# Kernel tuning notes

Measured on AMD Instinct MI355X. Metric: run time of the kernel, lower is better.

The kernel has to match this reference:

```python
import jax, jax.numpy as jnp
import numpy as np

NUM_CLASSES = 19
VIEWS = 50          # views_per_class: min(min_views, max_views_per_class)=50, no max_features_total cap (38*50<=10000)
TEMP = 0.1
CM_TEMP = 0.1
EPS = 1e-12


def setup_inputs() -> dict:
    key = jax.random.key(0)
    k1, k2, k3 = jax.random.split(key, 3)
    label = jax.random.randint(k1, (2, 512, 1024), 0, NUM_CLASSES)
    color_fea = jax.random.normal(k2, (2, 256, 128, 256), dtype=jnp.float32)
    other_fea = jax.random.normal(k3, (2, 256, 128, 256), dtype=jnp.float32)
    return {"label": label, "color_fea": color_fea, "other_fea": other_fea}


def _sample(compare, feature):
    # compare: [N, Cc, HW] bool (pixel belongs to class), feature: [N, C, HW]
    # random per-class sampling of VIEWS pixels: argsort random keys restricted to class pixels
    n, cc, hw = compare.shape
    rand = jax.random.uniform(jax.random.key(42), (n, hw))
    keys = jnp.where(compare, rand[:, None, :], 2.0)          # non-class pixels pushed to the end
    idx = jnp.argsort(keys, axis=-1)[:, :, :VIEWS]            # [N, Cc, V]
    samp = jnp.take_along_axis(feature[:, None, :, :], idx[:, :, None, :], axis=-1)  # [N, Cc, C, V]
    c = feature.shape[1]
    return samp.reshape(n * cc, c, VIEWS)                     # [T, C, V]


def _norm_flat(feats):
    # feats: [T, C, V] -> l2-normalize over C, transpose, flatten to [T*V, C]
    f = feats / jnp.maximum(jnp.linalg.norm(feats, axis=1, keepdims=True), EPS)
    t, c, v = f.shape
    return jnp.transpose(f, (0, 2, 1)).reshape(t * v, c)


def _masks(labels_flat):
    m = (labels_flat[:, None] == labels_flat[None, :]).astype(jnp.float32)
    neg = 1.0 - m
    pos = m * (1.0 - jnp.eye(m.shape[0], dtype=m.dtype))      # exclude self from positives
    return pos, neg


def _infonce(dot, pos, neg):
    exp = jnp.exp(dot)
    neg_logits = (exp * neg).sum(1, keepdims=True)
    log_prob = dot - jnp.log(exp + neg_logits)
    pos_sums = pos.sum(1)
    norm = jnp.where(pos_sums > 0, pos_sums, 1.0)
    return -(((pos * log_prob).sum(1)) / norm).mean()


def reference(label, color_fea, other_fea):
    n, h, w = label.shape
    scale = w // color_fea.shape[-1]
    # nearest-neighbour downsample of label to feature resolution (torch interpolate 'nearest' with integer factor)
    ld = label[:, ::scale, ::scale].reshape(n, -1)                       # [N, HW]
    compare = ld[:, None, :] == jnp.arange(NUM_CLASSES)[None, :, None]   # [N, Cc, HW]
    cf = color_fea.reshape(n, color_fea.shape[1], -1)
    of = other_fea.reshape(n, other_fea.shape[1], -1)
    fc = _sample(compare, cf)                                            # [T, C, V]
    fo = _sample(compare, of)
    labels = jnp.tile(jnp.arange(NUM_CLASSES), n).astype(jnp.float32)    # [T]
    labels_flat = jnp.repeat(labels, VIEWS)                              # [T*V]
    pos, neg = _masks(labels_flat)
    fcf = _norm_flat(fc)
    fof = _norm_flat(fo)
    loss_cm = _infonce(fcf @ fof.T / CM_TEMP, pos, neg)
    loss_vis = _infonce(fcf @ fcf.T / TEMP, pos, neg)
    loss_aux = _infonce(fof @ fof.T / TEMP, pos, neg)
    return (loss_cm, loss_vis, loss_aux)
```

## Files before the change

### kernel.cpp

```cpp
#include <hip/hip_runtime.h>
#include <hip/hip_bf16.h>
#include <cstdint>
#include <cstddef>

#define HW    32768
#define NCLS  19
#define VIEWS 50
#define NT    38
#define NR    1900
#define NRP   1920
#define CH    256
#define CAP   3072

#define OFF_LD   65536u
#define OFF_SEL  131072u
#define OFF_CNT  133120u
#define OFF_KEYS 133184u
#define OFF_FCF  366656u
#define OFF_FOF  612416u
#define OFF_NEG  858176u
#define OFF_POS  863936u

typedef __attribute__((ext_vector_type(8))) short short8;
typedef __attribute__((ext_vector_type(4))) float f32x4;

__device__ __forceinline__ unsigned rotl32(unsigned x, int d) {
    return (x << d) | (x >> (32 - d));
}

__device__ __forceinline__ void async_copy16(const void* g, void* l) {
    __builtin_amdgcn_global_load_lds(
        (const __attribute__((address_space(1))) unsigned int*)g,
        (__attribute__((address_space(3))) unsigned int*)l, 16, 0, 0);
}

__global__ __launch_bounds__(256) void prep_kernel(const int* __restrict__ label,
                                                   int* __restrict__ ld,
                                                   int* __restrict__ counts,
                                                   unsigned long long* __restrict__ keys,
                                                   float* __restrict__ negsum,
                                                   float* __restrict__ out) {
    int tid = threadIdx.x;
    int j = blockIdx.x * 256 + tid;
    unsigned x0 = (unsigned)j, x1 = (unsigned)(j + HW);
    const unsigned ks0 = 0u, ks1 = 42u, ks2 = 0x1BD11BDAu ^ 0u ^ 42u;
    x0 += ks0; x1 += ks1;
#define TF_RND(r) { x0 += x1; x1 = rotl32(x1, r); x1 ^= x0; }
    TF_RND(13) TF_RND(15) TF_RND(26) TF_RND(6)   x0 += ks1; x1 += ks2 + 1u;
    TF_RND(17) TF_RND(29) TF_RND(16) TF_RND(24)  x0 += ks2; x1 += ks0 + 2u;
    TF_RND(13) TF_RND(15) TF_RND(26) TF_RND(6)   x0 += ks0; x1 += ks1 + 3u;
    TF_RND(17) TF_RND(29) TF_RND(16) TF_RND(24)  x0 += ks1; x1 += ks2 + 4u;
    TF_RND(13) TF_RND(15) TF_RND(26) TF_RND(6)   x0 += ks2; x1 += ks0 + 5u;
#undef TF_RND
    float r0 = __uint_as_float((x0 >> 9) | 0x3f800000u) - 1.0f;
    float r1 = __uint_as_float((x1 >> 9) | 0x3f800000u) - 1.0f;
    int y = j >> 8, x = j & 255;
    int off = (y << 2) * 1024 + (x << 2);
    int c0 = label[off];
    int c1 = label[512 * 1024 + off];
    ld[j]      = c0;
    ld[HW + j] = c1;
    if (j < 3 * NR) negsum[j] = 0.0f;
    if (j < 3) out[j] = 0.0f;

    __shared__ int lcnt[NT], lbase[NT];
    if (tid < NT) lcnt[tid] = 0;
    __syncthreads();
    int t0 = c0, t1 = NCLS + c1;
    int p0 = atomicAdd(&lcnt[t0], 1);
    int p1 = atomicAdd(&lcnt[t1], 1);
    __syncthreads();
    if (tid < NT) {
        int c = lcnt[tid];
        lbase[tid] = (c > 0) ? atomicAdd(&counts[tid], c) : 0;
    }
    __syncthreads();
    int s0 = lbase[t0] + p0;
    int s1 = lbase[t1] + p1;
    if (s0 < CAP)
        keys[(size_t)t0 * CAP + s0] = (((unsigned long long)__float_as_uint(r0)) << 32) | (unsigned)j;
    if (s1 < CAP)
        keys[(size_t)t1 * CAP + s1] = (((unsigned long long)__float_as_uint(r1)) << 32) | (unsigned)j;
}

__global__ __launch_bounds__(256) void select_kernel(const int* __restrict__ counts,
                                                     const unsigned long long* __restrict__ keys,
                                                     const int* __restrict__ ld,
                                                     int* __restrict__ sel) {
    int t = blockIdx.x;
    int tid = threadIdx.x;
    int cnt = min(counts[t], CAP);
    const unsigned long long* g = keys + (size_t)t * CAP;
    __shared__ unsigned hist[256];
    __shared__ unsigned long long cand[256];
    __shared__ int s_B, s_nbelow, s_ncand;
    hist[tid] = 0;
    if (tid == 0) { s_B = 256; s_nbelow = 0; s_ncand = 0; }
    __syncthreads();

    unsigned long long kreg[12];
    int binreg[12];
    int nk = 0;
    for (int p = tid; p < cnt; p += 256) {
        unsigned long long k = g[p];
        unsigned v = (unsigned)(__uint_as_float((unsigned)(k >> 32)) * 8388608.0f);
        int b = (int)(v >> 15);
        kreg[nk] = k; binreg[nk] = b; nk++;
        atomicAdd(&hist[b], 1u);
    }
    __syncthreads();

    if (cnt >= VIEWS) {
        for (int s = 1; s < 256; s <<= 1) {
            unsigned add = (tid >= s) ? hist[tid - s] : 0u;
            unsigned cur = hist[tid];
            __syncthreads();
            hist[tid] = cur + add;
            __syncthreads();
        }
        unsigned cum  = hist[tid];
        unsigned prev = (tid > 0) ? hist[tid - 1] : 0u;
        if (cum >= VIEWS && prev < VIEWS) s_B = tid;
        __syncthreads();
        int B = s_B;
        for (int q = 0; q < nk; ++q) {
            if (binreg[q] < B) {
                int pos = atomicAdd(&s_nbelow, 1);
                if (pos < VIEWS) sel[t * VIEWS + pos] = (int)(kreg[q] & 0xffffffffu);
            } else if (binreg[q] == B) {
                int pos = atomicAdd(&s_ncand, 1);
                if (pos < 256) cand[pos] = kreg[q];
            }
        }
        __syncthreads();
        int nbelow = s_nbelow;
        int need   = VIEWS - nbelow;
        int ncand  = min(s_ncand, 256);
        if (tid < 64) {
            unsigned long long r0 = (tid       < ncand) ? cand[tid]       : ~0ull;
            unsigned long long r1 = (tid + 64  < ncand) ? cand[tid + 64]  : ~0ull;
            unsigned long long r2 = (tid + 128 < ncand) ? cand[tid + 128] : ~0ull;
            unsigned long long r3 = (tid + 192 < ncand) ? cand[tid + 192] : ~0ull;
            for (int v = 0; v < need; ++v) {
                unsigned long long a = (r0 < r1) ? r0 : r1;
                unsigned long long b = (r2 < r3) ? r2 : r3;
                unsigned long long best = (a < b) ? a : b;
                for (int m = 32; m >= 1; m >>= 1) {
                    unsigned long long o = __shfl_xor(best, m);
                    if (o < best) best = o;
                }
                if (tid == 0) sel[t * VIEWS + nbelow + v] = (int)(best & 0xffffffffu);
                if (r0 == best) r0 = ~0ull;
                if (r1 == best) r1 = ~0ull;
                if (r2 == best) r2 = ~0ull;
                if (r3 == best) r3 = ~0ull;
            }
        }
    } else {
        for (int q = 0; q < nk; ++q) {
            int pos = atomicAdd(&s_nbelow, 1);
            if (pos < VIEWS) sel[t * VIEWS + pos] = (int)(kreg[q] & 0xffffffffu);
        }
        __syncthreads();
        if (tid == 0) {
            int fill = s_nbelow;
            int n = t / NCLS, c = t % NCLS;
            const int* ldn = ld + n * HW;
            for (int j = 0; j < HW && fill < VIEWS; ++j)
                if (ldn[j] != c) sel[t * VIEWS + fill++] = j;
        }
    }
}

__global__ __launch_bounds__(256) void gather_kernel(const float* __restrict__ cf,
                                                     const float* __restrict__ of,
                                                     const int* __restrict__ sel,
                                                     unsigned short* __restrict__ fcf,
                                                     unsigned short* __restrict__ fof) {
    int r = blockIdx.x;
    int ch = threadIdx.x;
    if (r >= NR) {
        fcf[r * CH + ch] = 0;
        fof[r * CH + ch] = 0;
        return;
    }
    int t = r / VIEWS;
    int n = t / NCLS;
    int idx = sel[r];
    float vc = cf[(size_t)(n * CH + ch) * HW + idx];
    float vo = of[(size_t)(n * CH + ch) * HW + idx];
    __shared__ float partc[4], parto[4];
    float sc = vc * vc, so = vo * vo;
    for (int m = 32; m >= 1; m >>= 1) {
        sc += __shfl_xor(sc, m);
        so += __shfl_xor(so, m);
    }
    int wave = ch >> 6, lane = ch & 63;
    if (lane == 0) { partc[wave] = sc; parto[wave] = so; }
    __syncthreads();
    float nc = fmaxf(sqrtf(partc[0] + partc[1] + partc[2] + partc[3]), 1e-12f);
    float no = fmaxf(sqrtf(parto[0] + parto[1] + parto[2] + parto[3]), 1e-12f);
    __hip_bfloat16 hc = __float2bfloat16(vc / nc);
    __hip_bfloat16 ho = __float2bfloat16(vo / no);
    fcf[r * CH + ch] = *(unsigned short*)&hc;
    fof[r * CH + ch] = *(unsigned short*)&ho;
}

__global__ __launch_bounds__(256) void gram_kernel(const unsigned short* __restrict__ fcf,
                                                   const unsigned short* __restrict__ fof,
                                                   float* __restrict__ negsum,
                                                   float* __restrict__ posdot) {
    int z = blockIdx.z;
    bool sym = (z >= 1);
    if (sym && blockIdx.y > blockIdx.x) return;
    bool mirror = sym && (blockIdx.y < blockIdx.x);
    const unsigned short* A = (z == 2) ? fof : fcf;
    const unsigned short* B = (z == 1) ? fcf : fof;
    int i0 = blockIdx.y * 64, j0 = blockIdx.x * 64;
    int tid = threadIdx.x;
    int wave = tid >> 6, lane = tid & 63;
    __shared__ unsigned short As[64][32], Bs[64][32];
    __shared__ float negs[64], negsB[64];
    if (tid < 64) { negs[tid] = 0.0f; negsB[tid] = 0.0f; }
    f32x4 acc[4] = {{0,0,0,0},{0,0,0,0},{0,0,0,0},{0,0,0,0}};
    int srow = wave * 16 + (lane >> 2);
    int scol = (lane & 3) * 8;
    const unsigned short* ga = A + (size_t)(i0 + srow) * CH + scol;
    const unsigned short* gb = B + (size_t)(j0 + srow) * CH + scol;
    unsigned short* la = &As[wave * 16][0];
    unsigned short* lb = &Bs[wave * 16][0];
    int arow = wave * 16 + (lane & 15);
    int koff = (lane >> 4) * 8;
    for (int kc = 0; kc < CH; kc += 32) {
        async_copy16(ga + kc, la);
        async_copy16(gb + kc, lb);
        __syncthreads();
        short8 af = *(const short8*)&As[arow][koff];
        for (int b = 0; b < 4; ++b) {
            short8 bf = *(const short8*)&Bs[b * 16 + (lane & 15)][koff];
            acc[b] = __builtin_amdgcn_mfma_f32_16x16x32_bf16(af, bf, acc[b], 0, 0, 0);
        }
        __syncthreads();
    }
    float* pd = posdot + (size_t)z * NR * 100;
    int col = lane & 15, quad = lane >> 4;
    float negB[4] = {0.0f, 0.0f, 0.0f, 0.0f};
    for (int r = 0; r < 4; ++r) {
        int irow = wave * 16 + quad * 4 + r;
        int i = i0 + irow;
        bool iok = (i < NR);
        int ci = (i / VIEWS) % NCLS;
        float negacc = 0.0f;
        for (int b = 0; b < 4; ++b) {
            int j = j0 + b * 16 + col;
            if (!iok || j >= NR) continue;
            int cj = (j / VIEWS) % NCLS;
            float d = acc[b][r] * 10.0f;
            if (ci == cj) {
                int p = (j / (NCLS * VIEWS)) * VIEWS + (j % VIEWS);
                pd[(size_t)i * 100 + p] = d;
                if (mirror) {
                    int q = (i / (NCLS * VIEWS)) * VIEWS + (i % VIEWS);
                    pd[(size_t)j * 100 + q] = d;
                }
            } else {
                float e = __expf(d);
                negacc += e;
                if (mirror) negB[b] += e;
            }
        }
        for (int m = 8; m >= 1; m >>= 1) negacc += __shfl_xor(negacc, m);
        if (col == 0 && iok) negs[irow] = negacc;
    }
    if (mirror) {
        for (int b = 0; b < 4; ++b) {
            float v = negB[b];
            v += __shfl_xor(v, 16);
            v += __shfl_xor(v, 32);
            if (quad == 0) atomicAdd(&negsB[b * 16 + col], v);
        }
    }
    __syncthreads();
    if (tid < 64) {
        int i = i0 + tid;
        if (i < NR) atomicAdd(&negsum[z * NR + i], negs[tid]);
        if (mirror) {
            int j = j0 + tid;
            if (j < NR) atomicAdd(&negsum[z * NR + j], negsB[tid]);
        }
    }
}

__global__ void finalize_kernel(const float* __restrict__ negsum,
                                const float* __restrict__ posdot,
                                float* __restrict__ out) {
    int g = blockIdx.x * 256 + threadIdx.x;
    __shared__ float part[3];
    if (threadIdx.x < 3) part[threadIdx.x] = 0.0f;
    __syncthreads();
    if (g < 3 * NR) {
        int l = g / NR, i = g % NR;
        float NL = negsum[l * NR + i];
        int pself = (i / (NCLS * VIEWS)) * VIEWS + (i % VIEWS);
        const float* pd = posdot + ((size_t)l * NR + i) * 100;
        float s = 0.0f;
        for (int p = 0; p < 100; ++p) {
            if (p == pself) continue;
            float d = pd[p];
            s += d - logf(__expf(d) + NL);
        }
        atomicAdd(&part[l], s);
    }
    __syncthreads();
    if (threadIdx.x < 3)
        atomicAdd(&out[threadIdx.x], -part[threadIdx.x] * (1.0f / (99.0f * 1900.0f)));
}

extern "C" void kernel_launch(void* const* d_in, const int* in_sizes, int n_in,
                              void* d_out, int out_size, void* d_ws, size_t ws_size,
                              hipStream_t stream) {
    (void)in_sizes; (void)n_in; (void)out_size; (void)ws_size;
    const int*   label = (const int*)d_in[0];
    const float* cf    = (const float*)d_in[1];
    const float* of    = (const float*)d_in[2];
    float* ws = (float*)d_ws;
    int*                ld     = (int*)(ws + OFF_LD);
    int*                sel    = (int*)(ws + OFF_SEL);
    int*                counts = (int*)(ws + OFF_CNT);
    unsigned long long* keys   = (unsigned long long*)(ws + OFF_KEYS);
    unsigned short*     fcf    = (unsigned short*)(ws + OFF_FCF);
    unsigned short*     fof    = (unsigned short*)(ws + OFF_FOF);
    float*              negsum = ws + OFF_NEG;
    float*              posdot = ws + OFF_POS;
    float*              out    = (float*)d_out;

    hipMemsetAsync(counts, 0, NT * sizeof(int), stream);

    prep_kernel<<<HW / 256, 256, 0, stream>>>(label, ld, counts, keys, negsum, out);
    select_kernel<<<NT, 256, 0, stream>>>(counts, keys, ld, sel);
    gather_kernel<<<NRP, 256, 0, stream>>>(cf, of, sel, fcf, fof);
    dim3 g4(NRP / 64, NRP / 64, 3);
    gram_kernel<<<g4, 256, 0, stream>>>(fcf, fof, negsum, posdot);
    finalize_kernel<<<(3 * NR + 255) / 256, 256, 0, stream>>>(negsum, posdot, out);
}
```

Baseline: 205.0 us.

## Load full-K tiles into registers and padded LDS, remove per-chunk syncs

The gram kernel no longer streams 32-wide K chunks through LDS with async global-to-LDS copies and two barriers per chunk. Each wave now loads its whole A fragment (all 256 channels) straight into registers, and the B tile is staged once into a padded LDS array (row stride 272 to reduce bank conflicts), followed by a single barrier and a fully unrolled MFMA loop. This is meant to remove the per-iteration synchronisation and load latency stalls. In exchange it raises register and LDS use per block, which may lower occupancy.

```diff
diff --git a/kernel.cpp b/kernel.cpp
--- a/kernel.cpp
+++ b/kernel.cpp
@@ -26,12 +26,6 @@
 
 __device__ __forceinline__ unsigned rotl32(unsigned x, int d) {
     return (x << d) | (x >> (32 - d));
-}
-
-__device__ __forceinline__ void async_copy16(const void* g, void* l) {
-    __builtin_amdgcn_global_load_lds(
-        (const __attribute__((address_space(1))) unsigned int*)g,
-        (__attribute__((address_space(3))) unsigned int*)l, 16, 0, 0);
 }
 
 __global__ __launch_bounds__(256) void prep_kernel(const int* __restrict__ label,
@@ -206,6 +200,7 @@
     fof[r * CH + ch] = *(unsigned short*)&ho;
 }
 
+#define BLDS 272
 __global__ __launch_bounds__(256) void gram_kernel(const unsigned short* __restrict__ fcf,
                                                    const unsigned short* __restrict__ fof,
                                                    float* __restrict__ negsum,
@@ -219,29 +214,39 @@
     int i0 = blockIdx.y * 64, j0 = blockIdx.x * 64;
     int tid = threadIdx.x;
     int wave = tid >> 6, lane = tid & 63;
-    __shared__ unsigned short As[64][32], Bs[64][32];
+    __shared__ unsigned short Bs[64][BLDS];
     __shared__ float negs[64], negsB[64];
     if (tid < 64) { negs[tid] = 0.0f; negsB[tid] = 0.0f; }
+
+    short8 breg[8];
+#pragma unroll
+    for (int m = 0; m < 8; ++m) {
+        int e = m * 256 + tid;
+        int row = e >> 5, ch = (e & 31) * 8;
+        breg[m] = *(const short8*)(B + (size_t)(j0 + row) * CH + ch);
+    }
+    const unsigned short* pa = A + (size_t)(i0 + wave * 16 + (lane & 15)) * CH + (lane >> 4) * 8;
+    short8 af[8];
+#pragma unroll
+    for (int k = 0; k < 8; ++k) af[k] = *(const short8*)(pa + k * 32);
+#pragma unroll
+    for (int m = 0; m < 8; ++m) {
+        int e = m * 256 + tid;
+        int row = e >> 5, ch = (e & 31) * 8;
+        *(short8*)&Bs[row][ch] = breg[m];
+    }
+    __syncthreads();
+
     f32x4 acc[4] = {{0,0,0,0},{0,0,0,0},{0,0,0,0},{0,0,0,0}};
-    int srow = wave * 16 + (lane >> 2);
-    int scol = (lane & 3) * 8;
-    const unsigned short* ga = A + (size_t)(i0 + srow) * CH + scol;
-    const unsigned short* gb = B + (size_t)(j0 + srow) * CH + scol;
-    unsigned short* la = &As[wave * 16][0];
-    unsigned short* lb = &Bs[wave * 16][0];
-    int arow = wave * 16 + (lane & 15);
-    int koff = (lane >> 4) * 8;
-    for (int kc = 0; kc < CH; kc += 32) {
-        async_copy16(ga + kc, la);
-        async_copy16(gb + kc, lb);
-        __syncthreads();
-        short8 af = *(const short8*)&As[arow][koff];
+#pragma unroll
+    for (int k = 0; k < 8; ++k) {
+#pragma unroll
         for (int b = 0; b < 4; ++b) {
-            short8 bf = *(const short8*)&Bs[b * 16 + (lane & 15)][koff];
-            acc[b] = __builtin_amdgcn_mfma_f32_16x16x32_bf16(af, bf, acc[b], 0, 0, 0);
-        }
-        __syncthreads();
-    }
+            short8 bf = *(const short8*)&Bs[b * 16 + (lane & 15)][k * 32 + (lane >> 4) * 8];
+            acc[b] = __builtin_amdgcn_mfma_f32_16x16x32_bf16(af[k], bf, acc[b], 0, 0, 0);
+        }
+    }
+
     float* pd = posdot + (size_t)z * NR * 100;
     int col = lane & 15, quad = lane >> 4;
     float negB[4] = {0.0f, 0.0f, 0.0f, 0.0f};
```

After: 204.3 us. Within noise of the previous version (-0.3%).
